# Performance work log

Measured on AMD Instinct MI355X. Metric: run time of the kernel, lower is better.

The kernel has to match this reference:

```python
import jax, jax.numpy as jnp
import numpy as np

N_HEADS = 16
D_EMBED = 1024
D_CROSS = 768
D_HEAD = D_EMBED // N_HEADS
B, S = 4, 2048


def setup_inputs() -> dict:
    key = jax.random.key(0)
    ks = jax.random.split(key, 10)
    sq = lambda k, shp, fan: jax.random.normal(k, shp, jnp.float32) / np.sqrt(fan)
    return {
        "x": jax.random.normal(ks[0], (B, S, D_EMBED), jnp.float32),
        "y": jax.random.normal(ks[1], (B, S, D_CROSS), jnp.float32),
        "Wq": sq(ks[2], (D_EMBED, D_EMBED), D_EMBED),
        "bq": jnp.zeros((D_EMBED,), jnp.float32),
        "Wk": sq(ks[3], (D_CROSS, D_EMBED), D_CROSS),
        "bk": jnp.zeros((D_EMBED,), jnp.float32),
        "Wv": sq(ks[4], (D_CROSS, D_EMBED), D_CROSS),
        "bv": jnp.zeros((D_EMBED,), jnp.float32),
        "Wo": sq(ks[5], (D_EMBED, D_EMBED), D_EMBED),
        "bo": jnp.zeros((D_EMBED,), jnp.float32),
    }


def reference(x, y, Wq, bq, Wk, bk, Wv, bv, Wo, bo):
    b, s, _ = y.shape
    q = x @ Wq + bq  # [b, s, d_embed]
    k = y @ Wk + bk
    v = y @ Wv + bv
    # [b, h, s, d_head]
    q = q.reshape(b, s, N_HEADS, D_HEAD).transpose(0, 2, 1, 3)
    k = k.reshape(b, s, N_HEADS, D_HEAD).transpose(0, 2, 1, 3)
    v = v.reshape(b, s, N_HEADS, D_HEAD).transpose(0, 2, 1, 3)
    scale = 1.0 / np.sqrt(D_HEAD).astype(np.float32)
    scores = jnp.einsum("bhqd,bhkd->bhqk", q, k) * scale
    weights = jax.nn.softmax(scores, axis=-1)
    out = jnp.einsum("bhqk,bhkd->bhqd", weights, v)
    out = out.transpose(0, 2, 1, 3).reshape(x.shape)
    return out @ Wo + bo
```

## Files before the change

### kernel.cpp

```cpp
#include <hip/hip_runtime.h>

#define NHEADS 16
#define DEMBED 1024
#define DCROSS 768
#define DHEAD  64
#define BATCH  4
#define SLEN   2048
#define MROWS  (BATCH * SLEN)

using bf16   = __bf16;
using bf16x8 = __attribute__((ext_vector_type(8))) __bf16;
using bf16x4 = __attribute__((ext_vector_type(4))) __bf16;
using f32x4  = __attribute__((ext_vector_type(4))) float;

__device__ __forceinline__ f32x4 mfma_bf16(bf16x8 a, bf16x8 b, f32x4 c) {
    return __builtin_amdgcn_mfma_f32_16x16x32_bf16(a, b, c, 0, 0, 0);
}

__device__ __forceinline__ void gl2lds16(const void* g, void* l) {
    __builtin_amdgcn_global_load_lds(
        (const __attribute__((address_space(1))) void*)g,
        (__attribute__((address_space(3))) void*)l, 16, 0, 0);
}

struct PrepArgs {
    const float* wsrc[4]; bf16* wdst[4]; int wK[4];
    const float *x, *y; bf16 *xb, *yb;
};
#define NTRB 4096
__global__ void prep_all(PrepArgs a) {
    const int bid = blockIdx.x;
    const int tid = threadIdx.x;
    if (bid < NTRB) {
        __shared__ float tile[32][33];
        const int which = bid >> 10, rem = bid & 1023;
        const int K = a.wK[which], N = DEMBED;
        const int n0 = (rem & 31) * 32, k0 = (rem >> 5) * 32;
        if (k0 >= K) return;
        const float* W = a.wsrc[which];
        bf16* Wt = a.wdst[which];
        const int tx = tid & 31, ty = tid >> 5;
#pragma unroll
        for (int i = 0; i < 32; i += 8)
            tile[ty + i][tx] = W[(size_t)(k0 + ty + i) * N + n0 + tx];
        __syncthreads();
#pragma unroll
        for (int i = 0; i < 32; i += 8)
            Wt[(size_t)(n0 + ty + i) * K + k0 + tx] = (bf16)tile[tx][ty + i];
    } else {
        const int n4x = MROWS * DEMBED / 4;
        const int n4y = MROWS * DCROSS / 4;
        int i = (bid - NTRB) * 256 + tid;
        const float* src; bf16* dst; int j;
        if (i < n4x) { src = a.x; dst = a.xb; j = i; }
        else { j = i - n4x; if (j >= n4y) return; src = a.y; dst = a.yb; }
        float4 v = ((const float4*)src)[j];
        bf16x4 o = { (bf16)v.x, (bf16)v.y, (bf16)v.z, (bf16)v.w };
        ((bf16x4*)dst)[j] = o;
    }
}

struct QkvArgs {
    const bf16 *xb, *yb, *Wqt, *Wkt, *Wvt;
    const float *bq, *bk, *bv;
    bf16 *Qb, *Kb, *Vt;
    float qscale;
};
__global__ __launch_bounds__(256, 3) void gemm_qkv(QkvArgs a) {
    __shared__ bf16 As[128 * 64];
    __shared__ bf16 Bs[128 * 64];
    const int id = blockIdx.x;
    const int cls = id >> 9;
    const bf16 *A, *Bt;
    const float* bias;
    int K, m0, n0;
    if (cls == 0) { int t = id;        m0 = (t >> 3) * 128; n0 = (t & 7) * 128;
                    A = a.xb;  Bt = a.Wqt; bias = a.bq; K = DEMBED; }
    else if (cls == 1) { int t = id - 512;  m0 = (t >> 3) * 128; n0 = (t & 7) * 128;
                    A = a.yb;  Bt = a.Wkt; bias = a.bk; K = DCROSS; }
    else { int t = id - 1024; m0 = (t >> 6) * 128; n0 = (t & 63) * 128;
                    A = a.Wvt; Bt = a.yb;  bias = a.bv; K = DCROSS; }

    const int tid  = threadIdx.x;
    const int wave = tid >> 6, lane = tid & 63;
    const int quad = lane >> 4, l15 = lane & 15;
    const int wr = wave >> 1, wc = wave & 1;

    const int srow = wave * 8 + (lane >> 3);
    const int scol = ((lane & 7) ^ (lane >> 3)) * 8;
    char* ldsA0 = (char*)As + wave * 1024;
    char* ldsB0 = (char*)Bs + wave * 1024;
    const bf16* gA0 = A + (size_t)(m0 + srow) * K + scol;
    const bf16* gB0 = Bt + (size_t)(n0 + srow) * K + scol;

    const int sw = l15 & 7;

    f32x4 acc[4][4] = {};

    for (int kt = 0; kt < K; kt += 64) {
        __syncthreads();
#pragma unroll
        for (int c = 0; c < 4; c++)
            gl2lds16(gA0 + (size_t)c * 32 * K + kt, ldsA0 + c * 4096);
#pragma unroll
        for (int c = 0; c < 4; c++)
            gl2lds16(gB0 + (size_t)c * 32 * K + kt, ldsB0 + c * 4096);
        __syncthreads();

#pragma unroll
        for (int kg = 0; kg < 2; kg++) {
            bf16x8 af[4], bfr[4];
#pragma unroll
            for (int i = 0; i < 4; i++)
                af[i] = *(const bf16x8*)((const char*)As +
                         (wr * 64 + i * 16 + l15) * 128 + (((kg * 4 + quad) ^ sw) * 16));
#pragma unroll
            for (int i = 0; i < 4; i++)
                bfr[i] = *(const bf16x8*)((const char*)Bs +
                         (wc * 64 + i * 16 + l15) * 128 + (((kg * 4 + quad) ^ sw) * 16));
#pragma unroll
            for (int fr = 0; fr < 4; fr++)
#pragma unroll
                for (int fc = 0; fc < 4; fc++)
                    acc[fr][fc] = mfma_bf16(af[fr], bfr[fc], acc[fr][fc]);
        }
    }

    if (cls < 2) {
        bf16* Cout = (cls == 0) ? a.Qb : a.Kb;
        const float alpha = (cls == 0) ? a.qscale : 1.0f;
#pragma unroll
        for (int fr = 0; fr < 4; fr++) {
            int row = m0 + wr * 64 + fr * 16 + quad * 4;
#pragma unroll
            for (int fc = 0; fc < 4; fc++) {
                int col = n0 + wc * 64 + fc * 16 + l15;
                float bv = bias[col];
#pragma unroll
                for (int r = 0; r < 4; r++)
                    Cout[(size_t)(row + r) * DEMBED + col] =
                        (bf16)((acc[fr][fc][r] + bv) * alpha);
            }
        }
    } else {
        const int b = n0 >> 11;
        const size_t bbase = (size_t)b * DEMBED * SLEN;
#pragma unroll
        for (int fr = 0; fr < 4; fr++) {
            int row = m0 + wr * 64 + fr * 16 + quad * 4;
#pragma unroll
            for (int fc = 0; fc < 4; fc++) {
                int col = n0 + wc * 64 + fc * 16 + l15;
                int s = col & (SLEN - 1);
#pragma unroll
                for (int r = 0; r < 4; r++)
                    a.Vt[bbase + (size_t)(row + r) * SLEN + s] =
                        (bf16)(acc[fr][fc][r] + bias[row + r]);
            }
        }
    }
}

__global__ __launch_bounds__(256, 3) void gemm_o(const bf16* __restrict__ A,
                                                 const bf16* __restrict__ Bt,
                                                 const float* __restrict__ bias,
                                                 float* __restrict__ Cout) {
    const int K = DEMBED, N = DEMBED;
    __shared__ bf16 As[128 * 64];
    __shared__ bf16 Bs[128 * 64];
    const int tid  = threadIdx.x;
    const int wave = tid >> 6, lane = tid & 63;
    const int quad = lane >> 4, l15 = lane & 15;
    const int m0 = blockIdx.x * 128, n0 = blockIdx.y * 128;
    const int wr = wave >> 1, wc = wave & 1;

    const int srow = wave * 8 + (lane >> 3);
    const int scol = ((lane & 7) ^ (lane >> 3)) * 8;
    char* ldsA0 = (char*)As + wave * 1024;
    char* ldsB0 = (char*)Bs + wave * 1024;
    const bf16* gA0 = A + (size_t)(m0 + srow) * K + scol;
    const bf16* gB0 = Bt + (size_t)(n0 + srow) * K + scol;

    const int sw = l15 & 7;

    f32x4 acc[4][4] = {};

    for (int kt = 0; kt < K; kt += 64) {
        __syncthreads();
#pragma unroll
        for (int c = 0; c < 4; c++)
            gl2lds16(gA0 + (size_t)c * 32 * K + kt, ldsA0 + c * 4096);
#pragma unroll
        for (int c = 0; c < 4; c++)
            gl2lds16(gB0 + (size_t)c * 32 * K + kt, ldsB0 + c * 4096);
        __syncthreads();

#pragma unroll
        for (int kg = 0; kg < 2; kg++) {
            bf16x8 af[4], bfr[4];
#pragma unroll
            for (int i = 0; i < 4; i++)
                af[i] = *(const bf16x8*)((const char*)As +
                         (wr * 64 + i * 16 + l15) * 128 + (((kg * 4 + quad) ^ sw) * 16));
#pragma unroll
            for (int i = 0; i < 4; i++)
                bfr[i] = *(const bf16x8*)((const char*)Bs +
                         (wc * 64 + i * 16 + l15) * 128 + (((kg * 4 + quad) ^ sw) * 16));
#pragma unroll
            for (int fr = 0; fr < 4; fr++)
#pragma unroll
                for (int fc = 0; fc < 4; fc++)
                    acc[fr][fc] = mfma_bf16(af[fr], bfr[fc], acc[fr][fc]);
        }
    }

#pragma unroll
    for (int fr = 0; fr < 4; fr++) {
        int row = m0 + wr * 64 + fr * 16 + quad * 4;
#pragma unroll
        for (int fc = 0; fc < 4; fc++) {
            int col = n0 + wc * 64 + fc * 16 + l15;
            float bv = bias[col];
#pragma unroll
            for (int r = 0; r < 4; r++)
                Cout[(size_t)(row + r) * N + col] = acc[fr][fc][r] + bv;
        }
    }
}

__global__ __launch_bounds__(256, 4) void attn(const bf16* __restrict__ Q,
                                               const bf16* __restrict__ K,
                                               const bf16* __restrict__ Vt,
                                               bf16* __restrict__ O) {
    __shared__ bf16 KsA[64 * 64];
    __shared__ bf16 VsA[64 * 64];
    __shared__ bf16 PsA[4 * 32 * 72];

    const int tid  = threadIdx.x;
    const int wave = tid >> 6, lane = tid & 63;
    const int quad = lane >> 4, l15 = lane & 15;
    const int bh = blockIdx.x, b = bh >> 4, h = bh & 15;
    const size_t rowbase = (size_t)b * SLEN;
    const int qb = blockIdx.y * 128 + wave * 32;
    const int hc = h * DHEAD;

    bf16x8 qf[2][2];
#pragma unroll
    for (int rg = 0; rg < 2; rg++)
#pragma unroll
        for (int kg = 0; kg < 2; kg++)
            qf[rg][kg] = *(const bf16x8*)(Q + (rowbase + qb + rg * 16 + l15) * DEMBED
                                          + hc + kg * 32 + quad * 8);

    f32x4 o[2][4] = {};
    f32x4 lsv[2] = {};

    const bf16* Kbase = K + rowbase * DEMBED + hc;
    const bf16* Vbase = Vt + (size_t)bh * DHEAD * SLEN;

    const int xcol = (((tid & 7) ^ ((tid >> 3) & 7)) * 8);
    const bf16* gK = Kbase + (size_t)(tid >> 3) * DEMBED + xcol;
    const bf16* gV = Vbase + (size_t)(tid >> 3) * SLEN + xcol;
    char* ldsK = (char*)KsA + wave * 1024;
    char* ldsV = (char*)VsA + wave * 1024;
    bf16* Pw = PsA + wave * (32 * 72);

    for (int kb = 0; kb < SLEN; kb += 64) {
        __syncthreads();
        gl2lds16(gK + (size_t)kb * DEMBED, ldsK);
        gl2lds16(gK + (size_t)(kb + 32) * DEMBED, ldsK + 32 * 128);
        gl2lds16(gV + kb, ldsV);
        gl2lds16(gV + 32 * SLEN + kb, ldsV + 32 * 128);
        __syncthreads();

        f32x4 s[2][4] = {};
#pragma unroll
        for (int cg = 0; cg < 4; cg++)
#pragma unroll
            for (int kg = 0; kg < 2; kg++) {
                bf16x8 kf = *(const bf16x8*)((const char*)KsA +
                            (cg * 16 + l15) * 128 + (((kg * 4 + quad) ^ (l15 & 7)) * 16));
#pragma unroll
                for (int rg = 0; rg < 2; rg++)
                    s[rg][cg] = mfma_bf16(kf, qf[rg][kg], s[rg][cg]);
            }

#pragma unroll
        for (int rg = 0; rg < 2; rg++)
#pragma unroll
            for (int cg = 0; cg < 4; cg++) {
                f32x4 p;
                p[0] = __builtin_amdgcn_exp2f(s[rg][cg][0]);
                p[1] = __builtin_amdgcn_exp2f(s[rg][cg][1]);
                p[2] = __builtin_amdgcn_exp2f(s[rg][cg][2]);
                p[3] = __builtin_amdgcn_exp2f(s[rg][cg][3]);
                lsv[rg] += p;
                bf16x4 pb = { (bf16)p[0], (bf16)p[1], (bf16)p[2], (bf16)p[3] };
                *(bf16x4*)(Pw + (rg * 16 + l15) * 72 + cg * 16 + quad * 4) = pb;
            }

        bf16x8 ap[2][2];
#pragma unroll
        for (int rg = 0; rg < 2; rg++)
#pragma unroll
            for (int kg = 0; kg < 2; kg++)
                ap[rg][kg] = *(const bf16x8*)(Pw + (rg * 16 + l15) * 72 + kg * 32 + quad * 8);

#pragma unroll
        for (int dg = 0; dg < 4; dg++)
#pragma unroll
            for (int kg = 0; kg < 2; kg++) {
                bf16x8 vf = *(const bf16x8*)((const char*)VsA +
                            (dg * 16 + l15) * 128 + (((kg * 4 + quad) ^ (l15 & 7)) * 16));
#pragma unroll
                for (int rg = 0; rg < 2; rg++)
                    o[rg][dg] = mfma_bf16(ap[rg][kg], vf, o[rg][dg]);
            }
    }

    float inv[2];
#pragma unroll
    for (int rg = 0; rg < 2; rg++) {
        float rs = lsv[rg][0] + lsv[rg][1] + lsv[rg][2] + lsv[rg][3];
        rs += __shfl_xor(rs, 16);
        rs += __shfl_xor(rs, 32);
        inv[rg] = 1.0f / rs;
    }
#pragma unroll
    for (int rg = 0; rg < 2; rg++)
#pragma unroll
        for (int r = 0; r < 4; r++) {
            float iv = __shfl(inv[rg], quad * 4 + r);
#pragma unroll
            for (int dg = 0; dg < 4; dg++)
                O[(rowbase + qb + rg * 16 + quad * 4 + r) * DEMBED + hc + dg * 16 + l15] =
                    (bf16)(o[rg][dg][r] * iv);
        }
}

extern "C" void kernel_launch(void* const* d_in, const int* in_sizes, int n_in,
                              void* d_out, int out_size, void* d_ws, size_t ws_size,
                              hipStream_t stream) {
    const float* x  = (const float*)d_in[0];
    const float* y  = (const float*)d_in[1];
    const float* Wq = (const float*)d_in[2];
    const float* bq = (const float*)d_in[3];
    const float* Wk = (const float*)d_in[4];
    const float* bk = (const float*)d_in[5];
    const float* Wv = (const float*)d_in[6];
    const float* bv = (const float*)d_in[7];
    const float* Wo = (const float*)d_in[8];
    const float* bo = (const float*)d_in[9];
    float* out = (float*)d_out;

    char* ws = (char*)d_ws;
    size_t off = 0;
    auto alloc = [&](size_t bytes) {
        void* p = ws + off;
        off += (bytes + 255) & ~(size_t)255;
        return p;
    };
    bf16* xb  = (bf16*)alloc((size_t)MROWS * DEMBED * 2);
    bf16* yb  = (bf16*)alloc((size_t)MROWS * DCROSS * 2);
    bf16* Wqt = (bf16*)alloc((size_t)DEMBED * DEMBED * 2);
    bf16* Wkt = (bf16*)alloc((size_t)DEMBED * DCROSS * 2);
    bf16* Wvt = (bf16*)alloc((size_t)DEMBED * DCROSS * 2);
    bf16* Wot = (bf16*)alloc((size_t)DEMBED * DEMBED * 2);
    bf16* Qb  = (bf16*)alloc((size_t)MROWS * DEMBED * 2);
    bf16* Kb  = (bf16*)alloc((size_t)MROWS * DEMBED * 2);
    bf16* Vtb = (bf16*)alloc((size_t)MROWS * DEMBED * 2);
    bf16* Ab  = (bf16*)alloc((size_t)MROWS * DEMBED * 2);
    if (off > ws_size) return;

    {
        PrepArgs a;
        a.wsrc[0] = Wq; a.wdst[0] = Wqt; a.wK[0] = DEMBED;
        a.wsrc[1] = Wk; a.wdst[1] = Wkt; a.wK[1] = DCROSS;
        a.wsrc[2] = Wv; a.wdst[2] = Wvt; a.wK[2] = DCROSS;
        a.wsrc[3] = Wo; a.wdst[3] = Wot; a.wK[3] = DEMBED;
        a.x = x; a.y = y; a.xb = xb; a.yb = yb;
        int ncvt = (MROWS * DEMBED / 4 + MROWS * DCROSS / 4 + 255) / 256;
        prep_all<<<NTRB + ncvt, 256, 0, stream>>>(a);
    }

    {
        QkvArgs a;
        a.xb = xb; a.yb = yb; a.Wqt = Wqt; a.Wkt = Wkt; a.Wvt = Wvt;
        a.bq = bq; a.bk = bk; a.bv = bv;
        a.Qb = Qb; a.Kb = Kb; a.Vt = Vtb;
        a.qscale = 0.125f * 1.4426950408889634f;
        gemm_qkv<<<1536, 256, 0, stream>>>(a);
    }

    attn<<<dim3(BATCH * NHEADS, SLEN / 128), 256, 0, stream>>>(Qb, Kb, Vtb, Ab);

    gemm_o<<<dim3(MROWS / 128, DEMBED / 128), 256, 0, stream>>>(Ab, Wot, bo, out);
}
```

Before: 284.2 us.

## Rewrite attention inner loop with 32x32 MFMA, register P, and double-buffered K/V

The attention kernel now uses 32x32x16 bf16 MFMA tiles instead of 16x16x32. It transposes the probability tile through permlane32_swap in registers rather than a round trip through LDS. It also double-buffers the K/V LDS tiles so the next block loads while the current one is computed, with one barrier per iteration instead of two. This removes the P shared-memory traffic and the load stall, at the cost of twice the K/V LDS footprint and more accumulator registers.

```diff
diff --git a/kernel.cpp b/kernel.cpp
--- a/kernel.cpp
+++ b/kernel.cpp
@@ -11,10 +11,15 @@
 using bf16   = __bf16;
 using bf16x8 = __attribute__((ext_vector_type(8))) __bf16;
 using bf16x4 = __attribute__((ext_vector_type(4))) __bf16;
+using bf16x2 = __attribute__((ext_vector_type(2))) __bf16;
 using f32x4  = __attribute__((ext_vector_type(4))) float;
+using f32x16 = __attribute__((ext_vector_type(16))) float;
 
 __device__ __forceinline__ f32x4 mfma_bf16(bf16x8 a, bf16x8 b, f32x4 c) {
     return __builtin_amdgcn_mfma_f32_16x16x32_bf16(a, b, c, 0, 0, 0);
+}
+__device__ __forceinline__ f32x16 mfma32(bf16x8 a, bf16x8 b, f32x16 c) {
+    return __builtin_amdgcn_mfma_f32_32x32x16_bf16(a, b, c, 0, 0, 0);
 }
 
 __device__ __forceinline__ void gl2lds16(const void* g, void* l) {
@@ -232,28 +237,25 @@
                                                const bf16* __restrict__ K,
                                                const bf16* __restrict__ Vt,
                                                bf16* __restrict__ O) {
-    __shared__ bf16 KsA[64 * 64];
-    __shared__ bf16 VsA[64 * 64];
-    __shared__ bf16 PsA[4 * 32 * 72];
+    __shared__ bf16 KsA[2][64 * 64];
+    __shared__ bf16 VsA[2][64 * 64];
 
     const int tid  = threadIdx.x;
     const int wave = tid >> 6, lane = tid & 63;
-    const int quad = lane >> 4, l15 = lane & 15;
+    const int l31  = lane & 31, H = lane >> 5;
     const int bh = blockIdx.x, b = bh >> 4, h = bh & 15;
     const size_t rowbase = (size_t)b * SLEN;
     const int qb = blockIdx.y * 128 + wave * 32;
     const int hc = h * DHEAD;
 
-    bf16x8 qf[2][2];
-#pragma unroll
-    for (int rg = 0; rg < 2; rg++)
-#pragma unroll
-        for (int kg = 0; kg < 2; kg++)
-            qf[rg][kg] = *(const bf16x8*)(Q + (rowbase + qb + rg * 16 + l15) * DEMBED
-                                          + hc + kg * 32 + quad * 8);
-
-    f32x4 o[2][4] = {};
-    f32x4 lsv[2] = {};
+    bf16x8 qf[4];
+#pragma unroll
+    for (int ks = 0; ks < 4; ks++)
+        qf[ks] = *(const bf16x8*)(Q + (rowbase + qb + l31) * DEMBED
+                                  + hc + ks * 16 + H * 8);
+
+    f32x16 o[2] = {};
+    float lsv = 0.0f;
 
     const bf16* Kbase = K + rowbase * DEMBED + hc;
     const bf16* Vbase = Vt + (size_t)bh * DHEAD * SLEN;
@@ -261,81 +263,92 @@
     const int xcol = (((tid & 7) ^ ((tid >> 3) & 7)) * 8);
     const bf16* gK = Kbase + (size_t)(tid >> 3) * DEMBED + xcol;
     const bf16* gV = Vbase + (size_t)(tid >> 3) * SLEN + xcol;
-    char* ldsK = (char*)KsA + wave * 1024;
-    char* ldsV = (char*)VsA + wave * 1024;
-    bf16* Pw = PsA + wave * (32 * 72);
-
+
+    const int swz = l31 & 7;
+
+    {
+        char* lk = (char*)KsA + wave * 1024;
+        char* lv = (char*)VsA + wave * 1024;
+        gl2lds16(gK, lk);
+        gl2lds16(gK + (size_t)32 * DEMBED, lk + 32 * 128);
+        gl2lds16(gV, lv);
+        gl2lds16(gV + 32 * SLEN, lv + 32 * 128);
+    }
+    __syncthreads();
+
+    int cur = 0;
     for (int kb = 0; kb < SLEN; kb += 64) {
-        __syncthreads();
-        gl2lds16(gK + (size_t)kb * DEMBED, ldsK);
-        gl2lds16(gK + (size_t)(kb + 32) * DEMBED, ldsK + 32 * 128);
-        gl2lds16(gV + kb, ldsV);
-        gl2lds16(gV + 32 * SLEN + kb, ldsV + 32 * 128);
-        __syncthreads();
-
-        f32x4 s[2][4] = {};
-#pragma unroll
-        for (int cg = 0; cg < 4; cg++)
-#pragma unroll
-            for (int kg = 0; kg < 2; kg++) {
-                bf16x8 kf = *(const bf16x8*)((const char*)KsA +
-                            (cg * 16 + l15) * 128 + (((kg * 4 + quad) ^ (l15 & 7)) * 16));
-#pragma unroll
-                for (int rg = 0; rg < 2; rg++)
-                    s[rg][cg] = mfma_bf16(kf, qf[rg][kg], s[rg][cg]);
+        if (kb + 64 < SLEN) {
+            char* lk = (char*)KsA + (cur ^ 1) * 8192 + wave * 1024;
+            char* lv = (char*)VsA + (cur ^ 1) * 8192 + wave * 1024;
+            gl2lds16(gK + (size_t)(kb + 64) * DEMBED, lk);
+            gl2lds16(gK + (size_t)(kb + 96) * DEMBED, lk + 32 * 128);
+            gl2lds16(gV + kb + 64, lv);
+            gl2lds16(gV + 32 * SLEN + kb + 64, lv + 32 * 128);
+        }
+
+        const char* Kbuf = (const char*)KsA + cur * 8192;
+        const char* Vbuf = (const char*)VsA + cur * 8192;
+
+        f32x16 s0 = {}, s1 = {};
+#pragma unroll
+        for (int ks = 0; ks < 4; ks++) {
+            bf16x8 kf0 = *(const bf16x8*)(Kbuf + l31 * 128
+                          + (((2 * ks + H) ^ swz) * 16));
+            bf16x8 kf1 = *(const bf16x8*)(Kbuf + (32 + l31) * 128
+                          + (((2 * ks + H) ^ swz) * 16));
+            s0 = mfma32(kf0, qf[ks], s0);
+            s1 = mfma32(kf1, qf[ks], s1);
+        }
+
+        int c0[8], c1[8];
+#pragma unroll
+        for (int t = 0; t < 8; t++) {
+            float a0 = __builtin_amdgcn_exp2f(s0[2 * t]);
+            float a1 = __builtin_amdgcn_exp2f(s0[2 * t + 1]);
+            float b0 = __builtin_amdgcn_exp2f(s1[2 * t]);
+            float b1 = __builtin_amdgcn_exp2f(s1[2 * t + 1]);
+            lsv += (a0 + a1) + (b0 + b1);
+            union { bf16x2 h; int i; } p0, p1;
+            p0.h[0] = (bf16)a0; p0.h[1] = (bf16)a1;
+            p1.h[0] = (bf16)b0; p1.h[1] = (bf16)b1;
+            c0[t] = p0.i;
+            c1[t] = p1.i;
+        }
+
+#pragma unroll
+        for (int ks = 0; ks < 4; ks++) {
+            const int* cc = (ks < 2) ? c0 : c1;
+            const int ksl = ks & 1;
+            auto w0 = __builtin_amdgcn_permlane32_swap(cc[4 * ksl + 0],
+                                                       cc[4 * ksl + 2], false, false);
+            auto w1 = __builtin_amdgcn_permlane32_swap(cc[4 * ksl + 1],
+                                                       cc[4 * ksl + 3], false, false);
+            union { int i[4]; bf16x8 v; } ap;
+            ap.i[0] = w0[0]; ap.i[1] = w1[0]; ap.i[2] = w0[1]; ap.i[3] = w1[1];
+#pragma unroll
+            for (int dg = 0; dg < 2; dg++) {
+                bf16x8 vf = *(const bf16x8*)(Vbuf + (dg * 32 + l31) * 128
+                              + (((2 * ks + H) ^ swz) * 16));
+                o[dg] = mfma32(ap.v, vf, o[dg]);
             }
-
-#pragma unroll
-        for (int rg = 0; rg < 2; rg++)
-#pragma unroll
-            for (int cg = 0; cg < 4; cg++) {
-                f32x4 p;
-                p[0] = __builtin_amdgcn_exp2f(s[rg][cg][0]);
-                p[1] = __builtin_amdgcn_exp2f(s[rg][cg][1]);
-                p[2] = __builtin_amdgcn_exp2f(s[rg][cg][2]);
-                p[3] = __builtin_amdgcn_exp2f(s[rg][cg][3]);
-                lsv[rg] += p;
-                bf16x4 pb = { (bf16)p[0], (bf16)p[1], (bf16)p[2], (bf16)p[3] };
-                *(bf16x4*)(Pw + (rg * 16 + l15) * 72 + cg * 16 + quad * 4) = pb;
-            }
-
-        bf16x8 ap[2][2];
-#pragma unroll
-        for (int rg = 0; rg < 2; rg++)
-#pragma unroll
-            for (int kg = 0; kg < 2; kg++)
-                ap[rg][kg] = *(const bf16x8*)(Pw + (rg * 16 + l15) * 72 + kg * 32 + quad * 8);
-
-#pragma unroll
-        for (int dg = 0; dg < 4; dg++)
-#pragma unroll
-            for (int kg = 0; kg < 2; kg++) {
-                bf16x8 vf = *(const bf16x8*)((const char*)VsA +
-                            (dg * 16 + l15) * 128 + (((kg * 4 + quad) ^ (l15 & 7)) * 16));
-#pragma unroll
-                for (int rg = 0; rg < 2; rg++)
-                    o[rg][dg] = mfma_bf16(ap[rg][kg], vf, o[rg][dg]);
-            }
-    }
-
-    float inv[2];
-#pragma unroll
-    for (int rg = 0; rg < 2; rg++) {
-        float rs = lsv[rg][0] + lsv[rg][1] + lsv[rg][2] + lsv[rg][3];
-        rs += __shfl_xor(rs, 16);
-        rs += __shfl_xor(rs, 32);
-        inv[rg] = 1.0f / rs;
-    }
-#pragma unroll
-    for (int rg = 0; rg < 2; rg++)
-#pragma unroll
-        for (int r = 0; r < 4; r++) {
-            float iv = __shfl(inv[rg], quad * 4 + r);
-#pragma unroll
-            for (int dg = 0; dg < 4; dg++)
-                O[(rowbase + qb + rg * 16 + quad * 4 + r) * DEMBED + hc + dg * 16 + l15] =
-                    (bf16)(o[rg][dg][r] * iv);
-        }
+        }
+
+        __syncthreads();
+        cur ^= 1;
+    }
+
+    lsv += __shfl_xor(lsv, 32);
+    float inv = 1.0f / lsv;
+#pragma unroll
+    for (int r = 0; r < 16; r++) {
+        const int ql = (r & 3) + 8 * (r >> 2) + 4 * H;
+        float iv = __shfl(inv, ql);
+#pragma unroll
+        for (int dg = 0; dg < 2; dg++)
+            O[(rowbase + qb + ql) * DEMBED + hc + dg * 32 + l31] =
+                (bf16)(o[dg][r] * iv);
+    }
 }
 
 extern "C" void kernel_launch(void* const* d_in, const int* in_sizes, int n_in,
```

New measurement: 277.3 us. -2.4%, faster.
